# Performance work log

Measured on AMD Instinct MI355X. Metric: run time of the kernel, lower is better.

## Reference

```python
import jax, jax.numpy as jnp
import numpy as np

L, DIM = 8192, 2048

def setup_inputs() -> dict:
    key = jax.random.key(0)
    k1, k2, k3, k4 = jax.random.split(key, 4)
    x = jax.random.normal(k1, (L, DIM), dtype=jnp.float32)
    x_mix_last = jax.random.normal(k2, (DIM,), dtype=jnp.float32)
    factor_param = jax.random.uniform(k3, (DIM,), dtype=jnp.float32)
    W = jax.random.normal(k4, (DIM, DIM), dtype=jnp.float32) * 0.02
    return {"x": x, "x_mix_last": x_mix_last, "factor_param": factor_param, "W": W}

def reference(x, x_mix_last, factor_param, W):
    # x: [L, D] sequence-first, single sequence (no batch dim, as in the torch module)
    seq_len = x.shape[0]
    factor = jax.nn.sigmoid(factor_param)                       # [D]
    exps = jnp.arange(seq_len)[:, None]                         # [L, 1]
    factor_progression = factor[None, :] ** exps                # [L, D], factor^t
    n = 2 * seq_len
    # FFT-based causal convolution of x with the decay kernel factor^t
    fft_prog = jnp.fft.rfft(factor_progression, n=n, axis=0)    # [L+1, D] complex
    fft_x = jnp.fft.rfft(x, n=n, axis=0)                        # [L+1, D] complex
    conv = jnp.fft.irfft(fft_x * fft_prog, n=n, axis=0)[:seq_len]  # [L, D]
    # EMA update: carry decays as factor^(t+1), new input weighted by (1-factor)
    x_mix = x_mix_last[None, :] * factor_progression * factor[None, :] \
            + (1.0 - factor[None, :]) * conv                    # [L, D]
    return x_mix @ W.T                                          # nn.Linear: x @ W^T
```

## Files before the change

kernel.cpp:

```cpp
#include <hip/hip_runtime.h>

#define L_SEQ 8192
#define DIMN  2048
#define CHUNK 64
#define NCHUNK (L_SEQ / CHUNK)

typedef float  f32x4  __attribute__((ext_vector_type(4)));
typedef __bf16 bf16x8 __attribute__((ext_vector_type(8)));

__device__ __forceinline__ unsigned short f2bf(float f) {
    unsigned int u = __float_as_uint(f);
    u += 0x7fffu + ((u >> 16) & 1u);
    return (unsigned short)(u >> 16);
}

__device__ __forceinline__ float sigmoidf_(float v) {
    return 1.0f / (1.0f + __expf(-v));
}

__global__ void stage1(const float* __restrict__ x, const float* __restrict__ fp,
                       const float* __restrict__ W,
                       float* __restrict__ carry, unsigned short* __restrict__ Wb) {
    int b = blockIdx.x;
    if (b < 256) {
        int cg = b & 1;
        int c  = b >> 1;
        int d4 = cg * 256 + threadIdx.x;
        float4 f4 = ((const float4*)fp)[d4];
        float fa = sigmoidf_(f4.x), fb = sigmoidf_(f4.y),
              fc = sigmoidf_(f4.z), fd = sigmoidf_(f4.w);
        float ga = 1.f - fa, gb = 1.f - fb, gc = 1.f - fc, gd = 1.f - fd;
        float ha = 0.f, hb = 0.f, hc = 0.f, hd = 0.f;
        const float4* xp = (const float4*)(x + (size_t)c * CHUNK * DIMN) + d4;
#pragma unroll 8
        for (int t = 0; t < CHUNK; ++t) {
            float4 v = xp[(size_t)t * (DIMN / 4)];
            ha = fmaf(fa, ha, ga * v.x);
            hb = fmaf(fb, hb, gb * v.y);
            hc = fmaf(fc, hc, gc * v.z);
            hd = fmaf(fd, hd, gd * v.w);
        }
        ((float4*)(carry + (size_t)c * DIMN))[d4] = (float4){ha, hb, hc, hd};
    } else {
        int i = (b - 256) * 256 + threadIdx.x;
        float4 v = ((const float4*)W)[i];
        ushort4 o;
        o.x = f2bf(v.x); o.y = f2bf(v.y); o.z = f2bf(v.z); o.w = f2bf(v.w);
        ((ushort4*)Wb)[i] = o;
    }
}

__global__ __launch_bounds__(64) void carry_prefix(const float* __restrict__ fp,
                                                   const float* __restrict__ xml,
                                                   float* __restrict__ carry) {
    int d = blockIdx.x * 64 + threadIdx.x;
    float f = sigmoidf_(fp[d]);
    float fC = f;
    fC *= fC; fC *= fC; fC *= fC; fC *= fC; fC *= fC; fC *= fC;
    float v[NCHUNK];
#pragma unroll
    for (int c = 0; c < NCHUNK; ++c) v[c] = carry[(size_t)c * DIMN + d];
    float h = xml[d];
#pragma unroll
    for (int c = 0; c < NCHUNK; ++c) {
        carry[(size_t)c * DIMN + d] = h;
        h = fmaf(fC, h, v[c]);
    }
}

__global__ void scan_apply(const float* __restrict__ x, const float* __restrict__ fp,
                           const float* __restrict__ carry, unsigned short* __restrict__ xmix) {
    int b = blockIdx.x;
    int cg = b & 1;
    int c  = b >> 1;
    int d4 = cg * 256 + threadIdx.x;
    float4 f4 = ((const float4*)fp)[d4];
    float fa = sigmoidf_(f4.x), fb = sigmoidf_(f4.y),
          fc = sigmoidf_(f4.z), fd = sigmoidf_(f4.w);
    float ga = 1.f - fa, gb = 1.f - fb, gc = 1.f - fc, gd = 1.f - fd;
    float4 h0 = ((const float4*)(carry + (size_t)c * DIMN))[d4];
    float ha = h0.x, hb = h0.y, hc = h0.z, hd = h0.w;
    const float4* xp = (const float4*)(x + (size_t)c * CHUNK * DIMN) + d4;
    ushort4* op = (ushort4*)(xmix + (size_t)c * CHUNK * DIMN) + d4;
#pragma unroll 8
    for (int t = 0; t < CHUNK; ++t) {
        float4 v = xp[(size_t)t * (DIMN / 4)];
        ha = fmaf(fa, ha, ga * v.x);
        hb = fmaf(fb, hb, gb * v.y);
        hc = fmaf(fc, hc, gc * v.z);
        hd = fmaf(fd, hd, gd * v.w);
        ushort4 o; o.x = f2bf(ha); o.y = f2bf(hb); o.z = f2bf(hc); o.w = f2bf(hd);
        op[(size_t)t * (DIMN / 4)] = o;
    }
}

__global__ __launch_bounds__(256, 2) void gemm_bt(
        const unsigned short* __restrict__ A,
        const unsigned short* __restrict__ B,
        float* __restrict__ C) {
    constexpr int N_ = DIMN, K_ = DIMN;
    constexpr int BK = 64;
    __shared__ __align__(16) unsigned short As[128 * BK];
    __shared__ __align__(16) unsigned short Bs[256 * BK];

    int tid  = threadIdx.x;
    int wave = tid >> 6;
    int lane = tid & 63;
    int quad = lane >> 4;
    int l16  = lane & 15;
    int tm = blockIdx.x, tn = blockIdx.y;
    int wm = wave >> 1, wn = wave & 1;

    f32x4 acc[4][8];
#pragma unroll
    for (int i = 0; i < 4; ++i)
#pragma unroll
        for (int j = 0; j < 8; ++j)
            acc[i][j] = (f32x4){0.f, 0.f, 0.f, 0.f};

    const unsigned short* aBase = A + (size_t)(tm * 128) * K_;
    const unsigned short* bBase = B + (size_t)(tn * 256) * K_;

    for (int k0 = 0; k0 < K_; k0 += BK) {
#pragma unroll
        for (int i = 0; i < 4; ++i) {
            int idx = i * 256 + tid;
            int row = idx >> 3, slot = idx & 7;
            int cc = slot ^ (row & 7);
            __builtin_amdgcn_global_load_lds(
                (const __attribute__((address_space(1))) void*)(aBase + (size_t)row * K_ + k0 + cc * 8),
                (__attribute__((address_space(3))) void*)(As + idx * 8), 16, 0, 0);
        }
#pragma unroll
        for (int i = 0; i < 8; ++i) {
            int idx = i * 256 + tid;
            int row = idx >> 3, slot = idx & 7;
            int cc = slot ^ (row & 7);
            __builtin_amdgcn_global_load_lds(
                (const __attribute__((address_space(1))) void*)(bBase + (size_t)row * K_ + k0 + cc * 8),
                (__attribute__((address_space(3))) void*)(Bs + idx * 8), 16, 0, 0);
        }
        __syncthreads();

#pragma unroll
        for (int kk = 0; kk < BK; kk += 32) {
            bf16x8 af[4], bg[8];
#pragma unroll
            for (int i = 0; i < 4; ++i) {
                int r = wm * 64 + i * 16 + l16;
                int c0 = (kk >> 3) + quad;
                af[i] = *(const bf16x8*)(As + r * BK + ((c0 ^ (r & 7)) << 3));
            }
#pragma unroll
            for (int j = 0; j < 8; ++j) {
                int r = wn * 128 + j * 16 + l16;
                int c0 = (kk >> 3) + quad;
                bg[j] = *(const bf16x8*)(Bs + r * BK + ((c0 ^ (r & 7)) << 3));
            }
#pragma unroll
            for (int i = 0; i < 4; ++i)
#pragma unroll
                for (int j = 0; j < 8; ++j)
                    acc[i][j] = __builtin_amdgcn_mfma_f32_16x16x32_bf16(af[i], bg[j], acc[i][j], 0, 0, 0);
        }
        __syncthreads();
    }

#pragma unroll
    for (int i = 0; i < 4; ++i) {
#pragma unroll
        for (int j = 0; j < 8; ++j) {
            int col = tn * 256 + wn * 128 + j * 16 + l16;
#pragma unroll
            for (int r = 0; r < 4; ++r) {
                int row = tm * 128 + wm * 64 + i * 16 + quad * 4 + r;
                C[(size_t)row * N_ + col] = acc[i][j][r];
            }
        }
    }
}

extern "C" void kernel_launch(void* const* d_in, const int* in_sizes, int n_in,
                              void* d_out, int out_size, void* d_ws, size_t ws_size,
                              hipStream_t stream) {
    const float* x   = (const float*)d_in[0];
    const float* xml = (const float*)d_in[1];
    const float* fp  = (const float*)d_in[2];
    const float* W   = (const float*)d_in[3];
    float* out = (float*)d_out;

    unsigned short* xmix = (unsigned short*)d_ws;
    unsigned short* Wb   = (unsigned short*)((char*)d_ws + (size_t)L_SEQ * DIMN * 2);
    float* carry = (float*)((char*)d_ws + (size_t)L_SEQ * DIMN * 2 + (size_t)DIMN * DIMN * 2);

    stage1<<<256 + DIMN * DIMN / 4 / 256, 256, 0, stream>>>(x, fp, W, carry, Wb);
    carry_prefix<<<DIMN / 64, 64, 0, stream>>>(fp, xml, carry);
    scan_apply<<<256, 256, 0, stream>>>(x, fp, carry, xmix);
    gemm_bt<<<dim3(L_SEQ / 128, DIMN / 256), 256, 0, stream>>>(xmix, Wb, out);
}
```

Measured before the change: 202.5 us.

## Rewrite GEMM as 256x256 tile with 8 waves and double-buffered LDS pipeline

Replaces the single-buffered 128x256 bf16 GEMM with a 256x256 block tile using 512 threads (8 waves), splitting each 64-wide K step into two 32-wide halves held in a double-buffered 128 KB LDS region. Global-to-LDS loads for upcoming K slices are issued between MFMA phases, with explicit vmcnt waits, barriers and setprio, so memory traffic overlaps with matrix math. The aim is to hide load latency and raise reuse per byte loaded. In exchange it uses far more LDS per block, which likely limits occupancy, and it depends on a fragile hand-written wait-count schedule.

Measured after the change: 206.3 us. Within noise of the previous version (+1.9%).

```diff
diff --git a/kernel.cpp b/kernel.cpp
--- a/kernel.cpp
+++ b/kernel.cpp
@@ -94,90 +94,164 @@
     }
 }
 
-__global__ __launch_bounds__(256, 2) void gemm_bt(
+#define GLD16(gp, lp) __builtin_amdgcn_global_load_lds( \
+        (const __attribute__((address_space(1))) void*)(gp), \
+        (__attribute__((address_space(3))) void*)(lp), 16, 0, 0)
+#define WAITV(N) asm volatile("s_waitcnt vmcnt(" #N ")" ::: "memory")
+
+__global__ __launch_bounds__(512, 2) void gemm_bt(
         const unsigned short* __restrict__ A,
         const unsigned short* __restrict__ B,
         float* __restrict__ C) {
     constexpr int N_ = DIMN, K_ = DIMN;
-    constexpr int BK = 64;
-    __shared__ __align__(16) unsigned short As[128 * BK];
-    __shared__ __align__(16) unsigned short Bs[256 * BK];
-
-    int tid  = threadIdx.x;
-    int wave = tid >> 6;
-    int lane = tid & 63;
-    int quad = lane >> 4;
-    int l16  = lane & 15;
-    int tm = blockIdx.x, tn = blockIdx.y;
-    int wm = wave >> 1, wn = wave & 1;
-
-    f32x4 acc[4][8];
-#pragma unroll
-    for (int i = 0; i < 4; ++i)
-#pragma unroll
-        for (int j = 0; j < 8; ++j)
-            acc[i][j] = (f32x4){0.f, 0.f, 0.f, 0.f};
-
-    const unsigned short* aBase = A + (size_t)(tm * 128) * K_;
+    constexpr int NT = K_ / 64;
+    __shared__ __align__(16) unsigned short lds[2 * 32768];
+
+    const int tid  = threadIdx.x;
+    const int wave = tid >> 6;
+    const int lane = tid & 63;
+    const int quad = lane >> 4;
+    const int l16  = lane & 15;
+    const int wm = wave >> 2;
+    const int wn = wave & 3;
+    const int tm = blockIdx.x, tn = blockIdx.y;
+
+    const int i0 = tid, i1 = 512 + tid;
+    const int r0 = i0 >> 2, s0 = i0 & 3;
+    const int r1 = i1 >> 2, s1 = i1 & 3;
+    const size_t src0 = (size_t)r0 * K_ + (size_t)((s0 ^ ((r0 >> 1) & 3)) * 8);
+    const size_t src1 = (size_t)r1 * K_ + (size_t)((s1 ^ ((r1 >> 1) & 3)) * 8);
+    const int dst0 = tid * 8;
+    const int dst1 = 4096 + tid * 8;
+
+    const unsigned short* aBase = A + (size_t)(tm * 256) * K_;
     const unsigned short* bBase = B + (size_t)(tn * 256) * K_;
 
-    for (int k0 = 0; k0 < K_; k0 += BK) {
+    int offA[2][4], offB[4];
+#pragma unroll
+    for (int ih = 0; ih < 2; ++ih)
 #pragma unroll
         for (int i = 0; i < 4; ++i) {
-            int idx = i * 256 + tid;
-            int row = idx >> 3, slot = idx & 7;
-            int cc = slot ^ (row & 7);
-            __builtin_amdgcn_global_load_lds(
-                (const __attribute__((address_space(1))) void*)(aBase + (size_t)row * K_ + k0 + cc * 8),
-                (__attribute__((address_space(3))) void*)(As + idx * 8), 16, 0, 0);
+            int r = wm * 128 + ih * 64 + i * 16 + l16;
+            offA[ih][i] = r * 32 + ((quad ^ ((r >> 1) & 3)) << 3);
         }
 #pragma unroll
-        for (int i = 0; i < 8; ++i) {
-            int idx = i * 256 + tid;
-            int row = idx >> 3, slot = idx & 7;
-            int cc = slot ^ (row & 7);
-            __builtin_amdgcn_global_load_lds(
-                (const __attribute__((address_space(1))) void*)(bBase + (size_t)row * K_ + k0 + cc * 8),
-                (__attribute__((address_space(3))) void*)(Bs + idx * 8), 16, 0, 0);
-        }
-        __syncthreads();
-
-#pragma unroll
-        for (int kk = 0; kk < BK; kk += 32) {
-            bf16x8 af[4], bg[8];
-#pragma unroll
-            for (int i = 0; i < 4; ++i) {
-                int r = wm * 64 + i * 16 + l16;
-                int c0 = (kk >> 3) + quad;
-                af[i] = *(const bf16x8*)(As + r * BK + ((c0 ^ (r & 7)) << 3));
+    for (int j = 0; j < 4; ++j) {
+        int r = wn * 64 + j * 16 + l16;
+        offB[j] = r * 32 + ((quad ^ ((r >> 1) & 3)) << 3);
+    }
+
+    f32x4 acc[2][4][4];
+#pragma unroll
+    for (int ih = 0; ih < 2; ++ih)
+#pragma unroll
+        for (int i = 0; i < 4; ++i)
+#pragma unroll
+            for (int j = 0; j < 4; ++j)
+                acc[ih][i][j] = (f32x4){0.f, 0.f, 0.f, 0.f};
+
+#define STAGE(ab, h, b, t) do { \
+        const unsigned short* _g = ((ab) ? bBase : aBase) + (size_t)(t) * 64 + (h) * 32; \
+        unsigned short* _l = lds + (b) * 32768 + ((h) * 2 + (ab)) * 8192; \
+        GLD16(_g + src0, _l + dst0); \
+        GLD16(_g + src1, _l + dst1); \
+    } while (0)
+
+    STAGE(0, 0, 0, 0);
+    STAGE(1, 0, 0, 0);
+    STAGE(0, 1, 0, 0);
+    STAGE(1, 1, 0, 0);
+    STAGE(0, 0, 1, 1);
+    STAGE(1, 0, 1, 1);
+    WAITV(8);
+    __builtin_amdgcn_s_barrier();
+    __builtin_amdgcn_sched_barrier(0);
+
+    bf16x8 bg[4];
+    for (int T = 0; T < NT; ++T) {
+        const int buf = T & 1;
+        const unsigned short* Aklo = lds + buf * 32768;
+        const unsigned short* Bklo = Aklo + 8192;
+        const unsigned short* Akhi = Aklo + 16384;
+        const unsigned short* Bkhi = Aklo + 24576;
+        bf16x8 af[4];
+
+#pragma unroll
+        for (int i = 0; i < 4; ++i) af[i] = *(const bf16x8*)(Aklo + offA[0][i]);
+#pragma unroll
+        for (int j = 0; j < 4; ++j) bg[j] = *(const bf16x8*)(Bklo + offB[j]);
+        if (T + 1 < NT) STAGE(0, 1, buf ^ 1, T + 1);
+        __builtin_amdgcn_s_barrier();
+        __builtin_amdgcn_s_setprio(1);
+#pragma unroll
+        for (int i = 0; i < 4; ++i)
+#pragma unroll
+            for (int j = 0; j < 4; ++j)
+                acc[0][i][j] = __builtin_amdgcn_mfma_f32_16x16x32_bf16(af[i], bg[j], acc[0][i][j], 0, 0, 0);
+        __builtin_amdgcn_s_setprio(0);
+        __builtin_amdgcn_s_barrier();
+
+#pragma unroll
+        for (int i = 0; i < 4; ++i) af[i] = *(const bf16x8*)(Aklo + offA[1][i]);
+        if (T + 1 < NT) STAGE(1, 1, buf ^ 1, T + 1);
+        __builtin_amdgcn_s_barrier();
+        __builtin_amdgcn_s_setprio(1);
+#pragma unroll
+        for (int i = 0; i < 4; ++i)
+#pragma unroll
+            for (int j = 0; j < 4; ++j)
+                acc[1][i][j] = __builtin_amdgcn_mfma_f32_16x16x32_bf16(af[i], bg[j], acc[1][i][j], 0, 0, 0);
+        __builtin_amdgcn_s_setprio(0);
+        if (T < NT - 1) { WAITV(8); } else { WAITV(0); }
+        __builtin_amdgcn_s_barrier();
+        __builtin_amdgcn_sched_barrier(0);
+
+#pragma unroll
+        for (int i = 0; i < 4; ++i) af[i] = *(const bf16x8*)(Akhi + offA[0][i]);
+#pragma unroll
+        for (int j = 0; j < 4; ++j) bg[j] = *(const bf16x8*)(Bkhi + offB[j]);
+        if (T + 2 < NT) STAGE(0, 0, buf, T + 2);
+        __builtin_amdgcn_s_barrier();
+        __builtin_amdgcn_s_setprio(1);
+#pragma unroll
+        for (int i = 0; i < 4; ++i)
+#pragma unroll
+            for (int j = 0; j < 4; ++j)
+                acc[0][i][j] = __builtin_amdgcn_mfma_f32_16x16x32_bf16(af[i], bg[j], acc[0][i][j], 0, 0, 0);
+        __builtin_amdgcn_s_setprio(0);
+        __builtin_amdgcn_s_barrier();
+
+#pragma unroll
+        for (int i = 0; i < 4; ++i) af[i] = *(const bf16x8*)(Akhi + offA[1][i]);
+        if (T + 2 < NT) STAGE(1, 0, buf, T + 2);
+        __builtin_amdgcn_s_barrier();
+        __builtin_amdgcn_s_setprio(1);
+#pragma unroll
+        for (int i = 0; i < 4; ++i)
+#pragma unroll
+            for (int j = 0; j < 4; ++j)
+                acc[1][i][j] = __builtin_amdgcn_mfma_f32_16x16x32_bf16(af[i], bg[j], acc[1][i][j], 0, 0, 0);
+        __builtin_amdgcn_s_setprio(0);
+        if (T < NT - 2)      { WAITV(8); }
+        else if (T == NT - 2) { WAITV(4); }
+        __builtin_amdgcn_s_barrier();
+        __builtin_amdgcn_sched_barrier(0);
+    }
+#undef STAGE
+
+#pragma unroll
+    for (int ih = 0; ih < 2; ++ih)
+#pragma unroll
+        for (int i = 0; i < 4; ++i)
+#pragma unroll
+            for (int j = 0; j < 4; ++j) {
+                int col = tn * 256 + wn * 64 + j * 16 + l16;
+#pragma unroll
+                for (int r = 0; r < 4; ++r) {
+                    int row = tm * 256 + wm * 128 + ih * 64 + i * 16 + quad * 4 + r;
+                    C[(size_t)row * N_ + col] = acc[ih][i][j][r];
+                }
             }
-#pragma unroll
-            for (int j = 0; j < 8; ++j) {
-                int r = wn * 128 + j * 16 + l16;
-                int c0 = (kk >> 3) + quad;
-                bg[j] = *(const bf16x8*)(Bs + r * BK + ((c0 ^ (r & 7)) << 3));
-            }
-#pragma unroll
-            for (int i = 0; i < 4; ++i)
-#pragma unroll
-                for (int j = 0; j < 8; ++j)
-                    acc[i][j] = __builtin_amdgcn_mfma_f32_16x16x32_bf16(af[i], bg[j], acc[i][j], 0, 0, 0);
-        }
-        __syncthreads();
-    }
-
-#pragma unroll
-    for (int i = 0; i < 4; ++i) {
-#pragma unroll
-        for (int j = 0; j < 8; ++j) {
-            int col = tn * 256 + wn * 128 + j * 16 + l16;
-#pragma unroll
-            for (int r = 0; r < 4; ++r) {
-                int row = tm * 128 + wm * 64 + i * 16 + quad * 4 + r;
-                C[(size_t)row * N_ + col] = acc[i][j][r];
-            }
-        }
-    }
 }
 
 extern "C" void kernel_launch(void* const* d_in, const int* in_sizes, int n_in,
@@ -196,5 +270,5 @@
     stage1<<<256 + DIMN * DIMN / 4 / 256, 256, 0, stream>>>(x, fp, W, carry, Wb);
     carry_prefix<<<DIMN / 64, 64, 0, stream>>>(fp, xml, carry);
     scan_apply<<<256, 256, 0, stream>>>(x, fp, carry, xmix);
-    gemm_bt<<<dim3(L_SEQ / 128, DIMN / 256), 256, 0, stream>>>(xmix, Wb, out);
-}
+    gemm_bt<<<dim3(L_SEQ / 256, DIMN / 256), 512, 0, stream>>>(xmix, Wb, out);
+}
```

## Fuse three scan stages into one cooperative kernel with grid syncs

Applied to the files above, without the earlier changes.

Merges the chunk-carry computation, weight conversion, carry prefix and scan-apply kernels into a single cooperative kernel with 768 blocks, separated by grid-wide barriers. This removes two kernel launches and their inter-launch gaps. The prefix stage now runs on only 8 blocks of 256 threads, which lowers its parallelism and leaves most of the grid idle at the barriers. The weight conversion uses a grid-stride loop, and cooperative launch requires every block to be resident at once.

Result: slower. 549.9 us (+171.6%).

```diff
diff --git a/kernel.cpp b/kernel.cpp
--- a/kernel.cpp
+++ b/kernel.cpp
@@ -1,4 +1,7 @@
 #include <hip/hip_runtime.h>
+#include <hip/hip_cooperative_groups.h>
+
+namespace cg = cooperative_groups;
 
 #define L_SEQ 8192
 #define DIMN  2048
@@ -18,14 +21,18 @@
     return 1.0f / (1.0f + __expf(-v));
 }
 
-__global__ void stage1(const float* __restrict__ x, const float* __restrict__ fp,
-                       const float* __restrict__ W,
-                       float* __restrict__ carry, unsigned short* __restrict__ Wb) {
-    int b = blockIdx.x;
+__global__ __launch_bounds__(256, 4) void scan_all(
+        const float* __restrict__ x, const float* __restrict__ fp,
+        const float* __restrict__ W, const float* __restrict__ xml,
+        float* __restrict__ carry, unsigned short* __restrict__ Wb,
+        unsigned short* __restrict__ xmix) {
+    const int b = blockIdx.x;
+    const int tid = threadIdx.x;
+
     if (b < 256) {
-        int cg = b & 1;
-        int c  = b >> 1;
-        int d4 = cg * 256 + threadIdx.x;
+        int cg_ = b & 1;
+        int c   = b >> 1;
+        int d4  = cg_ * 256 + tid;
         float4 f4 = ((const float4*)fp)[d4];
         float fa = sigmoidf_(f4.x), fb = sigmoidf_(f4.y),
               fc = sigmoidf_(f4.z), fd = sigmoidf_(f4.w);
@@ -42,55 +49,58 @@
         }
         ((float4*)(carry + (size_t)c * DIMN))[d4] = (float4){ha, hb, hc, hd};
     } else {
-        int i = (b - 256) * 256 + threadIdx.x;
-        float4 v = ((const float4*)W)[i];
-        ushort4 o;
-        o.x = f2bf(v.x); o.y = f2bf(v.y); o.z = f2bf(v.z); o.w = f2bf(v.w);
-        ((ushort4*)Wb)[i] = o;
-    }
-}
-
-__global__ __launch_bounds__(64) void carry_prefix(const float* __restrict__ fp,
-                                                   const float* __restrict__ xml,
-                                                   float* __restrict__ carry) {
-    int d = blockIdx.x * 64 + threadIdx.x;
-    float f = sigmoidf_(fp[d]);
-    float fC = f;
-    fC *= fC; fC *= fC; fC *= fC; fC *= fC; fC *= fC; fC *= fC;
-    float v[NCHUNK];
-#pragma unroll
-    for (int c = 0; c < NCHUNK; ++c) v[c] = carry[(size_t)c * DIMN + d];
-    float h = xml[d];
-#pragma unroll
-    for (int c = 0; c < NCHUNK; ++c) {
-        carry[(size_t)c * DIMN + d] = h;
-        h = fmaf(fC, h, v[c]);
-    }
-}
-
-__global__ void scan_apply(const float* __restrict__ x, const float* __restrict__ fp,
-                           const float* __restrict__ carry, unsigned short* __restrict__ xmix) {
-    int b = blockIdx.x;
-    int cg = b & 1;
-    int c  = b >> 1;
-    int d4 = cg * 256 + threadIdx.x;
-    float4 f4 = ((const float4*)fp)[d4];
-    float fa = sigmoidf_(f4.x), fb = sigmoidf_(f4.y),
-          fc = sigmoidf_(f4.z), fd = sigmoidf_(f4.w);
-    float ga = 1.f - fa, gb = 1.f - fb, gc = 1.f - fc, gd = 1.f - fd;
-    float4 h0 = ((const float4*)(carry + (size_t)c * DIMN))[d4];
-    float ha = h0.x, hb = h0.y, hc = h0.z, hd = h0.w;
-    const float4* xp = (const float4*)(x + (size_t)c * CHUNK * DIMN) + d4;
-    ushort4* op = (ushort4*)(xmix + (size_t)c * CHUNK * DIMN) + d4;
+        for (int i = (b - 256) * 256 + tid; i < DIMN * DIMN / 4; i += 512 * 256) {
+            float4 v = ((const float4*)W)[i];
+            ushort4 o;
+            o.x = f2bf(v.x); o.y = f2bf(v.y); o.z = f2bf(v.z); o.w = f2bf(v.w);
+            ((ushort4*)Wb)[i] = o;
+        }
+    }
+    __threadfence();
+    cg::this_grid().sync();
+
+    if (b < 8) {
+        int d = b * 256 + tid;
+        float f = sigmoidf_(fp[d]);
+        float fC = f;
+        fC *= fC; fC *= fC; fC *= fC; fC *= fC; fC *= fC; fC *= fC;
+        float h = xml[d];
+        for (int c0 = 0; c0 < NCHUNK; c0 += 32) {
+            float v[32];
+#pragma unroll
+            for (int k = 0; k < 32; ++k) v[k] = carry[(size_t)(c0 + k) * DIMN + d];
+#pragma unroll
+            for (int k = 0; k < 32; ++k) {
+                carry[(size_t)(c0 + k) * DIMN + d] = h;
+                h = fmaf(fC, h, v[k]);
+            }
+        }
+    }
+    __threadfence();
+    cg::this_grid().sync();
+
+    if (b < 256) {
+        int cg_ = b & 1;
+        int c   = b >> 1;
+        int d4  = cg_ * 256 + tid;
+        float4 f4 = ((const float4*)fp)[d4];
+        float fa = sigmoidf_(f4.x), fb = sigmoidf_(f4.y),
+              fc = sigmoidf_(f4.z), fd = sigmoidf_(f4.w);
+        float ga = 1.f - fa, gb = 1.f - fb, gc = 1.f - fc, gd = 1.f - fd;
+        float4 h0 = ((const float4*)(carry + (size_t)c * DIMN))[d4];
+        float ha = h0.x, hb = h0.y, hc = h0.z, hd = h0.w;
+        const float4* xp = (const float4*)(x + (size_t)c * CHUNK * DIMN) + d4;
+        ushort4* op = (ushort4*)(xmix + (size_t)c * CHUNK * DIMN) + d4;
 #pragma unroll 8
-    for (int t = 0; t < CHUNK; ++t) {
-        float4 v = xp[(size_t)t * (DIMN / 4)];
-        ha = fmaf(fa, ha, ga * v.x);
-        hb = fmaf(fb, hb, gb * v.y);
-        hc = fmaf(fc, hc, gc * v.z);
-        hd = fmaf(fd, hd, gd * v.w);
-        ushort4 o; o.x = f2bf(ha); o.y = f2bf(hb); o.z = f2bf(hc); o.w = f2bf(hd);
-        op[(size_t)t * (DIMN / 4)] = o;
+        for (int t = 0; t < CHUNK; ++t) {
+            float4 v = xp[(size_t)t * (DIMN / 4)];
+            ha = fmaf(fa, ha, ga * v.x);
+            hb = fmaf(fb, hb, gb * v.y);
+            hc = fmaf(fc, hc, gc * v.z);
+            hd = fmaf(fd, hd, gd * v.w);
+            ushort4 o; o.x = f2bf(ha); o.y = f2bf(hb); o.z = f2bf(hc); o.w = f2bf(hd);
+            op[(size_t)t * (DIMN / 4)] = o;
+        }
     }
 }
 
@@ -193,8 +203,9 @@
     unsigned short* Wb   = (unsigned short*)((char*)d_ws + (size_t)L_SEQ * DIMN * 2);
     float* carry = (float*)((char*)d_ws + (size_t)L_SEQ * DIMN * 2 + (size_t)DIMN * DIMN * 2);
 
-    stage1<<<256 + DIMN * DIMN / 4 / 256, 256, 0, stream>>>(x, fp, W, carry, Wb);
-    carry_prefix<<<DIMN / 64, 64, 0, stream>>>(fp, xml, carry);
-    scan_apply<<<256, 256, 0, stream>>>(x, fp, carry, xmix);
+    void* args[] = { (void*)&x, (void*)&fp, (void*)&W, (void*)&xml,
+                     (void*)&carry, (void*)&Wb, (void*)&xmix };
+    hipLaunchCooperativeKernel(reinterpret_cast<void*>(scan_all),
+                               dim3(768), dim3(256), args, 0, stream);
     gemm_bt<<<dim3(L_SEQ / 128, DIMN / 256), 256, 0, stream>>>(xmix, Wb, out);
 }
```
